# Performance work log

Hardware: AMD Instinct MI355X
Metric: run time of the kernel (lower is better)

Reference implementation:

```python
import jax, jax.numpy as jnp
import numpy as np

B, H, W, C = 4, 64, 64, 21
THETA_ALPHA, THETA_BETA, THETA_GAMMA = 160.0, 3.0, 3.0
NUM_ITER = 5


def setup_inputs() -> dict:
    key = jax.random.key(0)
    k1, k2 = jax.random.split(key)
    unary = jax.random.normal(k1, (B, H, W, C), dtype=jnp.float32)
    rgb = jax.random.uniform(k2, (B, H, W, 3), dtype=jnp.float32) * 255.0
    # learned params per build(): diagonal init for kernel weights, Potts (-I) for compatibility
    spatial_ker_weights = jnp.eye(C, dtype=jnp.float32)
    bilateral_ker_weights = jnp.eye(C, dtype=jnp.float32)
    compatibility_matrix = -jnp.eye(C, dtype=jnp.float32)
    return {
        "unary": unary,
        "rgb": rgb,
        "spatial_ker_weights": spatial_ker_weights,
        "bilateral_ker_weights": bilateral_ker_weights,
        "compatibility_matrix": compatibility_matrix,
    }


def _pairwise_sq(f):
    # f: [..., N, D] -> squared euclidean distances [..., N, N]
    s = jnp.sum(f * f, axis=-1)
    return s[..., :, None] + s[..., None, :] - 2.0 * jnp.einsum('...nd,...md->...nm', f, f)


def _crf_mean_field(unary, rgb, Ws, Wb, compat):
    N = H * W
    yy, xx = jnp.meshgrid(jnp.arange(H, dtype=jnp.float32),
                          jnp.arange(W, dtype=jnp.float32), indexing='ij')
    coords = jnp.stack([yy.ravel(), xx.ravel()], axis=-1)  # [N, 2]

    # exact Gaussian kernels (what the permutohedral high_dim_filter approximates)
    Ks = jnp.exp(-0.5 * _pairwise_sq(coords / THETA_GAMMA))           # [N, N] spatial
    feats = jnp.concatenate(
        [jnp.broadcast_to(coords / THETA_ALPHA, (B, N, 2)),
         rgb.reshape(B, N, 3) / THETA_BETA], axis=-1)                  # [B, N, 5]
    Kb = jnp.exp(-0.5 * _pairwise_sq(feats))                           # [B, N, N] bilateral

    # norm vals = filter applied to all-ones (same for every channel)
    s_norm = jnp.sum(Ks, axis=1)        # [N]
    b_norm = jnp.sum(Kb, axis=2)        # [B, N]

    u = jnp.transpose(unary.reshape(B, N, C), (0, 2, 1))  # [B, C, N] (matches (C,H,W) flatten)
    q = u
    for _ in range(NUM_ITER):
        p = jax.nn.softmax(q, axis=1)                                   # softmax over classes
        sp = jnp.einsum('nm,bcm->bcn', Ks, p) / s_norm                  # spatial filtering + norm
        bl = jnp.einsum('bnm,bcm->bcn', Kb, p) / b_norm[:, None, :]     # bilateral filtering + norm
        msg = jnp.einsum('ck,bkn->bcn', Ws, sp) + jnp.einsum('ck,bkn->bcn', Wb, bl)
        pairwise = jnp.einsum('ck,bkn->bcn', compat, msg)               # compatibility transform
        q = u - pairwise
    return jnp.transpose(q, (0, 2, 1)).reshape(B, H, W, C)


def reference(unary, rgb, spatial_ker_weights, bilateral_ker_weights, compatibility_matrix):
    return _crf_mean_field(unary, rgb, spatial_ker_weights,
                           bilateral_ker_weights, compatibility_matrix)
```

## Files before the change

kernel.cpp:

```cpp
#include <hip/hip_runtime.h>
#include <stdint.h>
#include <math.h>

#define BB 4
#define CC 21
#define NN 4096
#define NITER 5
#define PH 64
#define PCH 22
#define PROW 72
#define CWR 24

#define CS_COEF  (-0.08014972449383172f)
#define CBC_COEF (-2.8177637517362567e-05f)
#define SB_SCALE (0.28310726680985215f)

typedef _Float16 f16x8 __attribute__((ext_vector_type(8)));
typedef float f32x16 __attribute__((ext_vector_type(16)));
typedef uint32_t u32;
typedef uint32_t u32x4 __attribute__((ext_vector_type(4)));

static __device__ __forceinline__ u32 pk2(float a, float b) {
  return __builtin_bit_cast(u32, __builtin_amdgcn_cvt_pkrtz(a, b));
}
static __device__ __forceinline__ f16x8 mk8(u32 a, u32 b, u32 c, u32 d) {
  u32x4 t = {a, b, c, d};
  return __builtin_bit_cast(f16x8, t);
}

__global__ __launch_bounds__(512) void crf_prep(const float* __restrict__ Ws,
                                                const float* __restrict__ Wb,
                                                const float* __restrict__ Cm,
                                                float* __restrict__ CW) {
  const int t = threadIdx.x;
  if (t < 441) {
    const int c = t / 21, k = t % 21;
    float as = 0.f, ab = 0.f;
    for (int j = 0; j < 21; ++j) {
      as += Cm[c * 21 + j] * Ws[j * 21 + k];
      ab += Cm[c * 21 + j] * Wb[j * 21 + k];
    }
    CW[k * CWR + c] = as;
    CW[21 * CWR + k * CWR + c] = ab;
  }
}

__global__ __launch_bounds__(256) void crf_filter(const float* __restrict__ grec,
                                                  const _Float16* __restrict__ pB,
                                                  float* __restrict__ part,
                                                  int mlen, int nmc) {
  __shared__ float g_lds[2][PH * 4];
  __shared__ _Float16 p_lds[2][PCH * PROW];

  const int chunk = blockIdx.x, ng = blockIdx.y, b = blockIdx.z;
  const int tid = threadIdx.x;
  const int wave = tid >> 6, lane = tid & 63;
  const int c = lane & 31, h = lane >> 5;
  const int ce = (c < PCH) ? c : (PCH - 1);
  const int ntile = ng * 4 + wave;
  const int n = (ntile << 5) + c;
  const float xn = (float)(n & 63);
  const float yn = (float)(n >> 6);
  const float xh = xn - (float)(h << 3);

  const float* grecb = grec + (size_t)b * NN * 4;
  const _Float16* pBb = pB + (size_t)b * PCH * NN;
  const float4 gn = *(const float4*)(grecb + (size_t)n * 4);
  const float gr2 = 2.f * gn.x, gg2 = 2.f * gn.y, gb2 = 2.f * gn.z;

  f16x8 sxa[4];
  float cdx2v[32];
#pragma unroll
  for (int q = 0; q < 4; ++q) {
    u32 w[4];
#pragma unroll
    for (int jp = 0; jp < 4; ++jp) {
      const float d0 = xh - (float)(q * 16 + 2 * jp);
      const float d1 = d0 - 1.0f;
      w[jp] = pk2(__builtin_amdgcn_exp2f(CS_COEF * d0 * d0),
                  __builtin_amdgcn_exp2f(CS_COEF * d1 * d1));
      cdx2v[q * 8 + 2 * jp]     = CBC_COEF * d0 * d0;
      cdx2v[q * 8 + 2 * jp + 1] = CBC_COEF * d1 * d1;
    }
    sxa[q] = mk8(w[0], w[1], w[2], w[3]);
  }

  f32x16 accs, accb, rowacc;
#pragma unroll
  for (int r = 0; r < 16; ++r) { accs[r] = 0.f; accb[r] = 0.f; rowacc[r] = 0.f; }

  const int m_lo = chunk * mlen;
  const int phases = mlen / PH;

  const int pidx = tid - 64;
  const int pch = pidx >> 3, po = pidx & 7;
  float4 stv;
  {
    if (tid < 64) stv = *(const float4*)(grecb + (size_t)(m_lo + tid) * 4);
    else if (tid < 240) stv = *(const float4*)(pBb + (size_t)pch * NN + m_lo + po * 8);
  }

  for (int p = 0; p < phases; ++p) {
    const int bsel = p & 1;
    if (tid < 64) *(float4*)&g_lds[bsel][tid * 4] = stv;
    else if (tid < 240) *(float4*)&p_lds[bsel][pch * PROW + po * 8] = stv;
    __syncthreads();
    if (p + 1 < phases) {
      const int mb = m_lo + (p + 1) * PH;
      if (tid < 64) stv = *(const float4*)(grecb + (size_t)(mb + tid) * 4);
      else if (tid < 240) stv = *(const float4*)(pBb + (size_t)pch * NN + mb + po * 8);
    }

    const int row = (m_lo >> 6) + p;
    const float dy = yn - (float)row;
    const float dy2 = dy * dy;
    const float sy = __builtin_amdgcn_exp2f(CS_COEF * dy2);
    const float crow = fmaf(CBC_COEF, dy2, gn.w);

    const float* gbuf = g_lds[bsel];
    const _Float16* pbuf = p_lds[bsel];
#pragma unroll
    for (int s = 0; s < 4; ++s) {
      float kb[8];
#pragma unroll
      for (int j = 0; j < 8; ++j) {
        const int idx = s * 16 + (h << 3) + j;
        const float4 gm = *(const float4*)&gbuf[idx * 4];
        float t = cdx2v[s * 8 + j] + crow;
        t = fmaf(gr2, gm.x, t);
        t = fmaf(gg2, gm.y, t);
        t = fmaf(gb2, gm.z, t);
        kb[j] = __builtin_amdgcn_exp2f(t + gm.w);
      }
      const f16x8 Ab = mk8(pk2(kb[0], kb[1]), pk2(kb[2], kb[3]),
                           pk2(kb[4], kb[5]), pk2(kb[6], kb[7]));
      const f16x8 Bf = *(const f16x8*)&pbuf[ce * PROW + s * 16 + (h << 3)];
      rowacc = __builtin_amdgcn_mfma_f32_32x32x16_f16(sxa[s], Bf, rowacc, 0, 0, 0);
      accb = __builtin_amdgcn_mfma_f32_32x32x16_f16(Ab, Bf, accb, 0, 0, 0);
    }
#pragma unroll
    for (int r = 0; r < 16; ++r) {
      accs[r] = fmaf(sy, rowacc[r], accs[r]);
      rowacc[r] = 0.f;
    }
    __syncthreads();
  }

  if (c < PCH) {
    float* os = part + (((size_t)(chunk * BB + b) * 2) * PCH + c) * NN + (ntile << 5) + (h << 2);
    float* ob = os + (size_t)PCH * NN;
#pragma unroll
    for (int g4 = 0; g4 < 4; ++g4) {
      *(float4*)(os + g4 * 8) = make_float4(accs[4 * g4], accs[4 * g4 + 1],
                                            accs[4 * g4 + 2], accs[4 * g4 + 3]);
      *(float4*)(ob + g4 * 8) = make_float4(accb[4 * g4], accb[4 * g4 + 1],
                                            accb[4 * g4 + 2], accb[4 * g4 + 3]);
    }
  }
}

__global__ __launch_bounds__(256) void crf_update(const float* __restrict__ unary,
                                                  const float* __restrict__ rgb,
                                                  const float* __restrict__ CW,
                                                  const float* __restrict__ part,
                                                  float* __restrict__ grec,
                                                  _Float16* __restrict__ pB,
                                                  float* __restrict__ dout,
                                                  int first, int last, int nmc) {
  const int g = blockIdx.x * 256 + threadIdx.x;
  const int P = g >> 2, cg = g & 3;
  const int b = P >> 12, n = P & 4095;

  float pair[21];
#pragma unroll
  for (int c = 0; c < 21; ++c) pair[c] = 0.f;

  if (!first) {
    float dots[21], dotb[21];
#pragma unroll
    for (int c = 0; c < 21; ++c) { dots[c] = 0.f; dotb[c] = 0.f; }
    float sn = 0.f, bn = 0.f;
    const size_t cst = (size_t)BB * 2 * PCH * NN;
#pragma unroll
    for (int i = 0; i < 6; ++i) {
      const int k = cg + 4 * i;
      if (k > 21) continue;
      const float* ps = part + (((size_t)b * 2) * PCH + k) * NN + n;
      float s_ = 0.f, b_ = 0.f;
      for (int ch = 0; ch < nmc; ++ch) {
        s_ += ps[(size_t)ch * cst];
        b_ += ps[(size_t)ch * cst + (size_t)PCH * NN];
      }
      if (k == 21) {
        sn = s_; bn = b_;
      } else {
        const float* w = CW + (size_t)k * CWR;
        const float* v = CW + (size_t)(21 + k) * CWR;
        float wv[21], vv[21];
        *(float4*)&wv[0]  = *(const float4*)(w);
        *(float4*)&wv[4]  = *(const float4*)(w + 4);
        *(float4*)&wv[8]  = *(const float4*)(w + 8);
        *(float4*)&wv[12] = *(const float4*)(w + 12);
        *(float4*)&wv[16] = *(const float4*)(w + 16);
        wv[20] = w[20];
        *(float4*)&vv[0]  = *(const float4*)(v);
        *(float4*)&vv[4]  = *(const float4*)(v + 4);
        *(float4*)&vv[8]  = *(const float4*)(v + 8);
        *(float4*)&vv[12] = *(const float4*)(v + 12);
        *(float4*)&vv[16] = *(const float4*)(v + 16);
        vv[20] = v[20];
#pragma unroll
        for (int c = 0; c < 21; ++c) {
          dots[c] = fmaf(wv[c], s_, dots[c]);
          dotb[c] = fmaf(vv[c], b_, dotb[c]);
        }
      }
    }
    sn += __shfl_xor(sn, 1); sn += __shfl_xor(sn, 2);
    bn += __shfl_xor(bn, 1); bn += __shfl_xor(bn, 2);
    const float isn = 1.f / sn, ibn = 1.f / bn;
#pragma unroll
    for (int c = 0; c < 21; ++c) {
      float vv2 = fmaf(dots[c], isn, dotb[c] * ibn);
      vv2 += __shfl_xor(vv2, 1);
      vv2 += __shfl_xor(vv2, 2);
      pair[c] = vv2;
    }
  }

  if (cg == 0) {
    const float* up = unary + (size_t)P * CC;
    float q[21];
#pragma unroll
    for (int c = 0; c < 21; ++c) q[c] = up[c] - pair[c];

    if (last) {
      float* op = dout + (size_t)P * CC;
#pragma unroll
      for (int c = 0; c < 21; ++c) op[c] = q[c];
    }

    float mx = q[0];
#pragma unroll
    for (int c = 1; c < 21; ++c) mx = fmaxf(mx, q[c]);
    float e[21], s = 0.f;
#pragma unroll
    for (int c = 0; c < 21; ++c) { e[c] = __expf(q[c] - mx); s += e[c]; }
    const float is = 1.f / s;

    const float* rg = rgb + (size_t)P * 3;
    const float g0 = rg[0] * SB_SCALE, g1 = rg[1] * SB_SCALE, g2 = rg[2] * SB_SCALE;
    *(float4*)(grec + (size_t)P * 4) =
        make_float4(g0, g1, g2, -fmaf(g2, g2, fmaf(g1, g1, g0 * g0)));

    _Float16* pb = pB + (size_t)b * PCH * NN + n;
#pragma unroll
    for (int c = 0; c < 21; ++c) pb[(size_t)c * NN] = (_Float16)(e[c] * is);
    pb[(size_t)21 * NN] = (_Float16)1.0f;
  }
}

extern "C" void kernel_launch(void* const* d_in, const int* in_sizes, int n_in,
                              void* d_out, int out_size, void* d_ws, size_t ws_size,
                              hipStream_t stream) {
  const float* unary = (const float*)d_in[0];
  const float* rgb   = (const float*)d_in[1];
  const float* Ws    = (const float*)d_in[2];
  const float* Wb    = (const float*)d_in[3];
  const float* Cm    = (const float*)d_in[4];
  float* out = (float*)d_out;

  float* grec = (float*)d_ws;
  const size_t grec_bytes = (size_t)BB * NN * 4 * 4;
  _Float16* pB = (_Float16*)((char*)d_ws + grec_bytes);
  const size_t pB_bytes = (size_t)BB * PCH * NN * 2;

  int nmc = 8;
  const size_t cw_bytes = (size_t)2 * 21 * CWR * 4;
  while (nmc > 1 &&
         ws_size < grec_bytes + pB_bytes + cw_bytes + (size_t)nmc * BB * 2 * PCH * NN * 4)
    nmc >>= 1;
  const int mlen = NN / nmc;
  float* part = (float*)((char*)d_ws + grec_bytes + pB_bytes);
  float* CW = part + (size_t)nmc * BB * 2 * PCH * NN;

  crf_prep<<<dim3(1), dim3(512), 0, stream>>>(Ws, Wb, Cm, CW);
  crf_update<<<dim3(256), dim3(256), 0, stream>>>(unary, rgb, CW, part, grec, pB,
                                                  out, 1, 0, nmc);
  for (int it = 0; it < NITER; ++it) {
    crf_filter<<<dim3(nmc, 32, BB), dim3(256), 0, stream>>>(grec, pB, part, mlen, nmc);
    crf_update<<<dim3(256), dim3(256), 0, stream>>>(unary, rgb, CW, part, grec, pB,
                                                    out, 0, (it == NITER - 1) ? 1 : 0, nmc);
  }
}
```

Baseline: 320.3 us.

## Reduce filter partial sums with atomics into ping-pong buffers instead of per-chunk slabs

The filter kernel now atomically accumulates its per-chunk spatial and bilateral partial sums into a single buffer per iteration, replacing separate per-chunk slabs that the update kernel had to sum. The update kernel reads one value per element and zeroes the other ping-pong buffer for the next iteration. The chunk count is fixed at 8 and the workspace-size fallback is removed. The aim is to cut the update kernel's 8-way reduction reads and the partial-buffer footprint, at the cost of 8-way float atomic contention and a grid-stride zeroing pass. Atomic accumulation also makes the summation order nondeterministic.

```diff
diff --git a/kernel.cpp b/kernel.cpp
--- a/kernel.cpp
+++ b/kernel.cpp
@@ -10,6 +10,7 @@
 #define PCH 22
 #define PROW 72
 #define CWR 24
+#define MLEN 512
 
 #define CS_COEF  (-0.08014972449383172f)
 #define CBC_COEF (-2.8177637517362567e-05f)
@@ -47,8 +48,7 @@
 
 __global__ __launch_bounds__(256) void crf_filter(const float* __restrict__ grec,
                                                   const _Float16* __restrict__ pB,
-                                                  float* __restrict__ part,
-                                                  int mlen, int nmc) {
+                                                  float* __restrict__ part) {
   __shared__ float g_lds[2][PH * 4];
   __shared__ _Float16 p_lds[2][PCH * PROW];
 
@@ -89,8 +89,7 @@
 #pragma unroll
   for (int r = 0; r < 16; ++r) { accs[r] = 0.f; accb[r] = 0.f; rowacc[r] = 0.f; }
 
-  const int m_lo = chunk * mlen;
-  const int phases = mlen / PH;
+  const int m_lo = chunk * MLEN;
 
   const int pidx = tid - 64;
   const int pch = pidx >> 3, po = pidx & 7;
@@ -100,12 +99,12 @@
     else if (tid < 240) stv = *(const float4*)(pBb + (size_t)pch * NN + m_lo + po * 8);
   }
 
-  for (int p = 0; p < phases; ++p) {
+  for (int p = 0; p < MLEN / PH; ++p) {
     const int bsel = p & 1;
     if (tid < 64) *(float4*)&g_lds[bsel][tid * 4] = stv;
     else if (tid < 240) *(float4*)&p_lds[bsel][pch * PROW + po * 8] = stv;
     __syncthreads();
-    if (p + 1 < phases) {
+    if (p + 1 < MLEN / PH) {
       const int mb = m_lo + (p + 1) * PH;
       if (tid < 64) stv = *(const float4*)(grecb + (size_t)(mb + tid) * 4);
       else if (tid < 240) stv = *(const float4*)(pBb + (size_t)pch * NN + mb + po * 8);
@@ -147,14 +146,13 @@
   }
 
   if (c < PCH) {
-    float* os = part + (((size_t)(chunk * BB + b) * 2) * PCH + c) * NN + (ntile << 5) + (h << 2);
+    float* os = part + (((size_t)b * 2 + 0) * PCH + c) * NN + (ntile << 5);
     float* ob = os + (size_t)PCH * NN;
 #pragma unroll
-    for (int g4 = 0; g4 < 4; ++g4) {
-      *(float4*)(os + g4 * 8) = make_float4(accs[4 * g4], accs[4 * g4 + 1],
-                                            accs[4 * g4 + 2], accs[4 * g4 + 3]);
-      *(float4*)(ob + g4 * 8) = make_float4(accb[4 * g4], accb[4 * g4 + 1],
-                                            accb[4 * g4 + 2], accb[4 * g4 + 3]);
+    for (int r = 0; r < 16; ++r) {
+      const int nloc = (r & 3) + ((r >> 2) << 3) + (h << 2);
+      atomicAdd(os + nloc, accs[r]);
+      atomicAdd(ob + nloc, accb[r]);
     }
   }
 }
@@ -162,11 +160,12 @@
 __global__ __launch_bounds__(256) void crf_update(const float* __restrict__ unary,
                                                   const float* __restrict__ rgb,
                                                   const float* __restrict__ CW,
-                                                  const float* __restrict__ part,
+                                                  const float* __restrict__ pin,
+                                                  float* __restrict__ pzero,
                                                   float* __restrict__ grec,
                                                   _Float16* __restrict__ pB,
                                                   float* __restrict__ dout,
-                                                  int first, int last, int nmc) {
+                                                  int first, int last) {
   const int g = blockIdx.x * 256 + threadIdx.x;
   const int P = g >> 2, cg = g & 3;
   const int b = P >> 12, n = P & 4095;
@@ -180,17 +179,12 @@
 #pragma unroll
     for (int c = 0; c < 21; ++c) { dots[c] = 0.f; dotb[c] = 0.f; }
     float sn = 0.f, bn = 0.f;
-    const size_t cst = (size_t)BB * 2 * PCH * NN;
 #pragma unroll
     for (int i = 0; i < 6; ++i) {
       const int k = cg + 4 * i;
       if (k > 21) continue;
-      const float* ps = part + (((size_t)b * 2) * PCH + k) * NN + n;
-      float s_ = 0.f, b_ = 0.f;
-      for (int ch = 0; ch < nmc; ++ch) {
-        s_ += ps[(size_t)ch * cst];
-        b_ += ps[(size_t)ch * cst + (size_t)PCH * NN];
-      }
+      const float s_ = pin[(((size_t)b * 2 + 0) * PCH + k) * NN + n];
+      const float b_ = pin[(((size_t)b * 2 + 1) * PCH + k) * NN + n];
       if (k == 21) {
         sn = s_; bn = b_;
       } else {
@@ -258,6 +252,11 @@
     for (int c = 0; c < 21; ++c) pb[(size_t)c * NN] = (_Float16)(e[c] * is);
     pb[(size_t)21 * NN] = (_Float16)1.0f;
   }
+
+  const int PF4 = BB * 2 * PCH * NN / 4;
+  float4* pz = (float4*)pzero;
+  for (int j = g; j < PF4; j += 65536)
+    pz[j] = make_float4(0.f, 0.f, 0.f, 0.f);
 }
 
 extern "C" void kernel_launch(void* const* d_in, const int* in_sizes, int n_in,
@@ -271,25 +270,25 @@
   float* out = (float*)d_out;
 
   float* grec = (float*)d_ws;
-  const size_t grec_bytes = (size_t)BB * NN * 4 * 4;
-  _Float16* pB = (_Float16*)((char*)d_ws + grec_bytes);
-  const size_t pB_bytes = (size_t)BB * PCH * NN * 2;
-
-  int nmc = 8;
-  const size_t cw_bytes = (size_t)2 * 21 * CWR * 4;
-  while (nmc > 1 &&
-         ws_size < grec_bytes + pB_bytes + cw_bytes + (size_t)nmc * BB * 2 * PCH * NN * 4)
-    nmc >>= 1;
-  const int mlen = NN / nmc;
-  float* part = (float*)((char*)d_ws + grec_bytes + pB_bytes);
-  float* CW = part + (size_t)nmc * BB * 2 * PCH * NN;
+  const size_t grec_f = (size_t)BB * NN * 4;
+  _Float16* pB = (_Float16*)(grec + grec_f);
+  const size_t pB_f = (size_t)BB * PCH * NN;
+  float* CW = (float*)(pB + pB_f);
+  const size_t cw_f = (size_t)2 * 21 * CWR;
+  float* part0 = CW + cw_f;
+  const size_t part_f = (size_t)BB * 2 * PCH * NN;
+  float* part1 = part0 + part_f;
+  float* partbuf[2] = {part0, part1};
 
   crf_prep<<<dim3(1), dim3(512), 0, stream>>>(Ws, Wb, Cm, CW);
-  crf_update<<<dim3(256), dim3(256), 0, stream>>>(unary, rgb, CW, part, grec, pB,
-                                                  out, 1, 0, nmc);
+  crf_update<<<dim3(256), dim3(256), 0, stream>>>(unary, rgb, CW, part0, part0,
+                                                  grec, pB, out, 1, 0);
   for (int it = 0; it < NITER; ++it) {
-    crf_filter<<<dim3(nmc, 32, BB), dim3(256), 0, stream>>>(grec, pB, part, mlen, nmc);
-    crf_update<<<dim3(256), dim3(256), 0, stream>>>(unary, rgb, CW, part, grec, pB,
-                                                    out, 0, (it == NITER - 1) ? 1 : 0, nmc);
-  }
-}
+    crf_filter<<<dim3(8, 32, BB), dim3(256), 0, stream>>>(grec, pB, partbuf[it & 1]);
+    crf_update<<<dim3(256), dim3(256), 0, stream>>>(unary, rgb, CW,
+                                                    partbuf[it & 1],
+                                                    partbuf[(it + 1) & 1],
+                                                    grec, pB, out, 0,
+                                                    (it == NITER - 1) ? 1 : 0);
+  }
+}
```

Measured after the change: 868.9 us. +171.3%, slower.
